# Optimization experiments

Hardware: AMD Instinct MI355X
Metric: run time of the kernel (lower is better)

Reference implementation:

```python
import jax, jax.numpy as jnp
import numpy as np

THRESH = 1.0   # snntorch Leaky default threshold
SLOPE = 25.0   # surrogate.fast_sigmoid default slope
BETA = 0.92

@jax.custom_vjp
def spike_fn(x):
    # Heaviside forward, fast-sigmoid surrogate backward
    return (x > 0).astype(x.dtype)

def _spike_fwd(x):
    return spike_fn(x), x

def _spike_bwd(x, g):
    return (g / (SLOPE * jnp.abs(x) + 1.0) ** 2,)

spike_fn.defvjp(_spike_fwd, _spike_bwd)


def setup_inputs() -> dict:
    key = jax.random.key(0)
    ks = jax.random.split(key, 5)
    T, B, I, H, O = 1000, 8192, 9, 96, 3
    return {
        "spike_input": jax.random.uniform(ks[0], (T, B, I), dtype=jnp.float32),
        "W1": jax.random.normal(ks[1], (H, I), dtype=jnp.float32) * (1.0 / np.sqrt(I)),
        "b1": jax.random.normal(ks[2], (H,), dtype=jnp.float32) * 0.1,
        "W2": jax.random.normal(ks[3], (O, H), dtype=jnp.float32) * (1.0 / np.sqrt(H)),
        "b2": jax.random.normal(ks[4], (O,), dtype=jnp.float32) * 0.1,
    }


def reference(spike_input, W1, b1, W2, b2):
    T, B, _ = spike_input.shape
    H = W1.shape[0]
    O = W2.shape[0]
    mem1_0 = jnp.zeros((B, H), dtype=spike_input.dtype)
    mem2_0 = jnp.zeros((B, O), dtype=spike_input.dtype)

    def step(carry, x_t):
        mem1, mem2 = carry
        # layer 1: Linear + Leaky (subtract reset, reset uses detached spike of incoming mem)
        cur1 = x_t @ W1.T + b1
        rst1 = jax.lax.stop_gradient((mem1 > THRESH).astype(mem1.dtype))
        mem1 = BETA * mem1 + cur1 - rst1 * THRESH
        spk1 = spike_fn(mem1 - THRESH)
        # layer 2
        cur2 = spk1 @ W2.T + b2
        rst2 = jax.lax.stop_gradient((mem2 > THRESH).astype(mem2.dtype))
        mem2 = BETA * mem2 + cur2 - rst2 * THRESH
        spk2 = spike_fn(mem2 - THRESH)
        return (mem1, mem2), (spk2, mem2)

    _, (spk2_rec, mem2_rec) = jax.lax.scan(step, (mem1_0, mem2_0), spike_input)
    return spk2_rec, mem2_rec
```

## Files before the change

kernel.cpp:

```cpp
#include <hip/hip_runtime.h>


#define T_STEPS 1000
#define BATCH   8192
#define NIN     9
#define HID     96
#define NOUT    3
#define GRP     16
#define UPL     6

__device__ __forceinline__ void loadx(float xr[NIN], const float* __restrict__ p) {
    #pragma unroll
    for (int i = 0; i < NIN; ++i) xr[i] = p[i];
}

__global__ __launch_bounds__(256) void snn_fwd_kernel(
    const float* __restrict__ x,
    const float* __restrict__ W1,
    const float* __restrict__ b1,
    const float* __restrict__ W2,
    const float* __restrict__ b2,
    float* __restrict__ out)
{
    const int tid = blockIdx.x * blockDim.x + threadIdx.x;
    const int li  = tid & (GRP - 1);
    const int b   = tid >> 4;
    const int u0  = li * UPL;

    float w1r[UPL][NIN];
    float b1r[UPL];
    float w2r[NOUT][UPL];
    #pragma unroll
    for (int u = 0; u < UPL; ++u) {
        b1r[u] = b1[u0 + u];
        #pragma unroll
        for (int i = 0; i < NIN; ++i)
            w1r[u][i] = W1[(u0 + u) * NIN + i];
    }
    #pragma unroll
    for (int o = 0; o < NOUT; ++o)
        #pragma unroll
        for (int u = 0; u < UPL; ++u)
            w2r[o][u] = W2[o * HID + u0 + u];
    const float b2r0 = b2[0], b2r1 = b2[1], b2r2 = b2[2];

    float mem1[UPL], spk1[UPL];
    #pragma unroll
    for (int u = 0; u < UPL; ++u) { mem1[u] = 0.0f; spk1[u] = 0.0f; }
    float m20 = 0.0f, m21 = 0.0f, m22 = 0.0f;
    float s20 = 0.0f, s21 = 0.0f, s22 = 0.0f;

    const float* xrow = x + (size_t)b * NIN;
    const size_t xstride = (size_t)BATCH * NIN;

    const size_t ostride  = (size_t)BATCH * NOUT;
    const size_t mem_base = (size_t)T_STEPS * ostride;
    const size_t obase0   = (size_t)b * NOUT;

    float x0[NIN], x1[NIN], x2[NIN], x3[NIN];
    loadx(x0, xrow + 0 * xstride);
    loadx(x1, xrow + 1 * xstride);

    #define CLAMP_T(tt) (((tt) < T_STEPS) ? (tt) : (T_STEPS - 1))

    #define STEP(tcur, xr)                                                     \
    do {                                                                       \
             \
        float acc[UPL];                                                        \
        _Pragma("unroll")                                                      \
        for (int u = 0; u < UPL; ++u) acc[u] = 0.0f;                           \
        _Pragma("unroll")                                                      \
        for (int i = 0; i < NIN; ++i) {                                        \
            float xi = (xr)[i];                                                \
            _Pragma("unroll")                                                  \
            for (int u = 0; u < UPL; ++u)                                      \
                acc[u] = __builtin_fmaf(xi, w1r[u][i], acc[u]);                \
        }                                                                      \
                          \
        _Pragma("unroll")                                                      \
        for (int u = 0; u < UPL; ++u) {                                        \
            float cur = __fadd_rn(acc[u], b1r[u]);                             \
            float m = __fadd_rn(__fmul_rn(0.92f, mem1[u]), cur);               \
            m = __fsub_rn(m, spk1[u]);                                         \
            mem1[u] = m;                                                       \
            spk1[u] = (m > 1.0f) ? 1.0f : 0.0f;                                \
        }                                                                      \
                  \
        float p0, p1, p2;                                                      \
        {                                                                      \
            float s = 0.0f;                                                    \
            _Pragma("unroll")                                                  \
            for (int u = 0; u < UPL; ++u)                                      \
                s = __builtin_fmaf(spk1[u], w2r[0][u], s);                     \
            s = __fadd_rn(s, __shfl_xor(s, 1, GRP));                           \
            s = __fadd_rn(s, __shfl_xor(s, 2, GRP));                           \
            s = __fadd_rn(s, __shfl_xor(s, 4, GRP));                           \
            s = __fadd_rn(s, __shfl_xor(s, 8, GRP));                           \
            p0 = s;                                                            \
        }                                                                      \
        {                                                                      \
            float s = 0.0f;                                                    \
            _Pragma("unroll")                                                  \
            for (int u = 0; u < UPL; ++u)                                      \
                s = __builtin_fmaf(spk1[u], w2r[1][u], s);                     \
            s = __fadd_rn(s, __shfl_xor(s, 1, GRP));                           \
            s = __fadd_rn(s, __shfl_xor(s, 2, GRP));                           \
            s = __fadd_rn(s, __shfl_xor(s, 4, GRP));                           \
            s = __fadd_rn(s, __shfl_xor(s, 8, GRP));                           \
            p1 = s;                                                            \
        }                                                                      \
        {                                                                      \
            float s = 0.0f;                                                    \
            _Pragma("unroll")                                                  \
            for (int u = 0; u < UPL; ++u)                                      \
                s = __builtin_fmaf(spk1[u], w2r[2][u], s);                     \
            s = __fadd_rn(s, __shfl_xor(s, 1, GRP));                           \
            s = __fadd_rn(s, __shfl_xor(s, 2, GRP));                           \
            s = __fadd_rn(s, __shfl_xor(s, 4, GRP));                           \
            s = __fadd_rn(s, __shfl_xor(s, 8, GRP));                           \
            p2 = s;                                                            \
        }                                                                      \
                              \
        {                                                                      \
            float cur = __fadd_rn(p0, b2r0);                                   \
            float m = __fadd_rn(__fmul_rn(0.92f, m20), cur);                   \
            m = __fsub_rn(m, s20);                                             \
            m20 = m; s20 = (m > 1.0f) ? 1.0f : 0.0f;                           \
        }                                                                      \
        {                                                                      \
            float cur = __fadd_rn(p1, b2r1);                                   \
            float m = __fadd_rn(__fmul_rn(0.92f, m21), cur);                   \
            m = __fsub_rn(m, s21);                                             \
            m21 = m; s21 = (m > 1.0f) ? 1.0f : 0.0f;                           \
        }                                                                      \
        {                                                                      \
            float cur = __fadd_rn(p2, b2r2);                                   \
            float m = __fadd_rn(__fmul_rn(0.92f, m22), cur);                   \
            m = __fsub_rn(m, s22);                                             \
            m22 = m; s22 = (m > 1.0f) ? 1.0f : 0.0f;                           \
        }                                                                      \
                                  \
        const size_t ob = (size_t)(tcur) * ostride + obase0;                   \
        if (li < NOUT) {                                                       \
            float v = (li == 0) ? s20 : (li == 1) ? s21 : s22;                 \
            __builtin_nontemporal_store(v, &out[ob + li]);                     \
        } else if (li < 2 * NOUT) {                                            \
            int c = li - NOUT;                                                 \
            float v = (c == 0) ? m20 : (c == 1) ? m21 : m22;                   \
            __builtin_nontemporal_store(v, &out[mem_base + ob + c]);           \
        }                                                                      \
    } while (0)

    for (int t = 0; t < T_STEPS; t += 4) {
        loadx(x2, xrow + (size_t)CLAMP_T(t + 2) * xstride);
        STEP(t, x0);
        loadx(x3, xrow + (size_t)CLAMP_T(t + 3) * xstride);
        STEP(t + 1, x1);
        loadx(x0, xrow + (size_t)CLAMP_T(t + 4) * xstride);
        STEP(t + 2, x2);
        loadx(x1, xrow + (size_t)CLAMP_T(t + 5) * xstride);
        STEP(t + 3, x3);
    }
    #undef STEP
    #undef CLAMP_T
}

extern "C" void kernel_launch(void* const* d_in, const int* in_sizes, int n_in,
                              void* d_out, int out_size, void* d_ws, size_t ws_size,
                              hipStream_t stream) {
    const float* x  = (const float*)d_in[0];
    const float* W1 = (const float*)d_in[1];
    const float* b1 = (const float*)d_in[2];
    const float* W2 = (const float*)d_in[3];
    const float* b2 = (const float*)d_in[4];
    float* out = (float*)d_out;

    const int total_threads = BATCH * GRP;
    dim3 block(256);
    dim3 grid(total_threads / 256);
    snn_fwd_kernel<<<grid, block, 0, stream>>>(x, W1, b1, W2, b2, out);
}
```

Before: 946.5 us.

## Spread each batch row across 32 lanes and pair-exchange spikes before layer-2 reduction

Each batch element now uses 32 lanes with 3 hidden units per lane instead of 16 lanes with 6. Paired lanes swap their layer-1 spikes so each lane computes a 6-term partial dot product for layer 2, which drops one butterfly shuffle stage per output but adds three spike shuffles. Launch bounds now request 4 blocks per SM and the output stores become normal stores rather than nontemporal. Total thread count doubles, so every lane reloads the x row and recomputes the layer-2 reduction redundantly, in exchange for shorter per-lane serial dependency chains and more latency hiding.

```diff
diff --git a/kernel.cpp b/kernel.cpp
--- a/kernel.cpp
+++ b/kernel.cpp
@@ -6,15 +6,16 @@
 #define NIN     9
 #define HID     96
 #define NOUT    3
-#define GRP     16
-#define UPL     6
+#define GRP     32
+#define UPL     3
+#define CPL     6
 
 __device__ __forceinline__ void loadx(float xr[NIN], const float* __restrict__ p) {
     #pragma unroll
     for (int i = 0; i < NIN; ++i) xr[i] = p[i];
 }
 
-__global__ __launch_bounds__(256) void snn_fwd_kernel(
+__global__ __launch_bounds__(256, 4) void snn_fwd_kernel(
     const float* __restrict__ x,
     const float* __restrict__ W1,
     const float* __restrict__ b1,
@@ -24,12 +25,14 @@
 {
     const int tid = blockIdx.x * blockDim.x + threadIdx.x;
     const int li  = tid & (GRP - 1);
-    const int b   = tid >> 4;
+    const int b   = tid / GRP;
+    const int par = li & 1;
     const int u0  = li * UPL;
+    const int pb  = (li >> 1) * CPL;
 
     float w1r[UPL][NIN];
     float b1r[UPL];
-    float w2r[NOUT][UPL];
+    float w2r[NOUT][CPL];
     #pragma unroll
     for (int u = 0; u < UPL; ++u) {
         b1r[u] = b1[u0 + u];
@@ -40,8 +43,8 @@
     #pragma unroll
     for (int o = 0; o < NOUT; ++o)
         #pragma unroll
-        for (int u = 0; u < UPL; ++u)
-            w2r[o][u] = W2[o * HID + u0 + u];
+        for (int j = 0; j < CPL; ++j)
+            w2r[o][j] = W2[o * HID + pb + j];
     const float b2r0 = b2[0], b2r1 = b2[1], b2r2 = b2[2];
 
     float mem1[UPL], spk1[UPL];
@@ -65,7 +68,7 @@
 
     #define STEP(tcur, xr)                                                     \
     do {                                                                       \
-             \
+                        \
         float acc[UPL];                                                        \
         _Pragma("unroll")                                                      \
         for (int u = 0; u < UPL; ++u) acc[u] = 0.0f;                           \
@@ -85,39 +88,49 @@
             mem1[u] = m;                                                       \
             spk1[u] = (m > 1.0f) ? 1.0f : 0.0f;                                \
         }                                                                      \
-                  \
+              \
+        float spo[UPL];                                                        \
+        _Pragma("unroll")                                                      \
+        for (int u = 0; u < UPL; ++u) spo[u] = __shfl_xor(spk1[u], 1, GRP);    \
+        float spk6[CPL];                                                       \
+        _Pragma("unroll")                                                      \
+        for (int u = 0; u < UPL; ++u) {                                        \
+            spk6[u]       = par ? spo[u]  : spk1[u];                           \
+            spk6[u + UPL] = par ? spk1[u] : spo[u];                            \
+        }                                                                      \
+               \
         float p0, p1, p2;                                                      \
         {                                                                      \
             float s = 0.0f;                                                    \
             _Pragma("unroll")                                                  \
-            for (int u = 0; u < UPL; ++u)                                      \
-                s = __builtin_fmaf(spk1[u], w2r[0][u], s);                     \
-            s = __fadd_rn(s, __shfl_xor(s, 1, GRP));                           \
+            for (int j = 0; j < CPL; ++j)                                      \
+                s = __builtin_fmaf(spk6[j], w2r[0][j], s);                     \
             s = __fadd_rn(s, __shfl_xor(s, 2, GRP));                           \
             s = __fadd_rn(s, __shfl_xor(s, 4, GRP));                           \
             s = __fadd_rn(s, __shfl_xor(s, 8, GRP));                           \
+            s = __fadd_rn(s, __shfl_xor(s, 16, GRP));                          \
             p0 = s;                                                            \
         }                                                                      \
         {                                                                      \
             float s = 0.0f;                                                    \
             _Pragma("unroll")                                                  \
-            for (int u = 0; u < UPL; ++u)                                      \
-                s = __builtin_fmaf(spk1[u], w2r[1][u], s);                     \
-            s = __fadd_rn(s, __shfl_xor(s, 1, GRP));                           \
+            for (int j = 0; j < CPL; ++j)                                      \
+                s = __builtin_fmaf(spk6[j], w2r[1][j], s);                     \
             s = __fadd_rn(s, __shfl_xor(s, 2, GRP));                           \
             s = __fadd_rn(s, __shfl_xor(s, 4, GRP));                           \
             s = __fadd_rn(s, __shfl_xor(s, 8, GRP));                           \
+            s = __fadd_rn(s, __shfl_xor(s, 16, GRP));                          \
             p1 = s;                                                            \
         }                                                                      \
         {                                                                      \
             float s = 0.0f;                                                    \
             _Pragma("unroll")                                                  \
-            for (int u = 0; u < UPL; ++u)                                      \
-                s = __builtin_fmaf(spk1[u], w2r[2][u], s);                     \
-            s = __fadd_rn(s, __shfl_xor(s, 1, GRP));                           \
+            for (int j = 0; j < CPL; ++j)                                      \
+                s = __builtin_fmaf(spk6[j], w2r[2][j], s);                     \
             s = __fadd_rn(s, __shfl_xor(s, 2, GRP));                           \
             s = __fadd_rn(s, __shfl_xor(s, 4, GRP));                           \
             s = __fadd_rn(s, __shfl_xor(s, 8, GRP));                           \
+            s = __fadd_rn(s, __shfl_xor(s, 16, GRP));                          \
             p2 = s;                                                            \
         }                                                                      \
                               \
@@ -143,11 +156,11 @@
         const size_t ob = (size_t)(tcur) * ostride + obase0;                   \
         if (li < NOUT) {                                                       \
             float v = (li == 0) ? s20 : (li == 1) ? s21 : s22;                 \
-            __builtin_nontemporal_store(v, &out[ob + li]);                     \
+            out[ob + li] = v;                                                  \
         } else if (li < 2 * NOUT) {                                            \
             int c = li - NOUT;                                                 \
             float v = (c == 0) ? m20 : (c == 1) ? m21 : m22;                   \
-            __builtin_nontemporal_store(v, &out[mem_base + ob + c]);           \
+            out[mem_base + ob + c] = v;                                        \
         }                                                                      \
     } while (0)
 
```

New measurement: 1.132 ms. +19.6%, slower.
